# Performance work log

Measured on AMD Instinct MI355X. Metric: run time of the kernel, lower is better.

Reference implementation:

```python
import jax, jax.numpy as jnp
import numpy as np

N_NODES = 10000
N_EDGES = 640000
D_IN = 128
D_OUT = 128


def setup_inputs() -> dict:
    key = jax.random.key(0)
    ks = jax.random.split(key, 8)
    x = jax.random.normal(ks[0], (N_NODES, D_IN), dtype=jnp.float32)
    edge_index = jax.random.randint(ks[1], (2, N_EDGES), 0, N_NODES, dtype=jnp.int64)
    batch = jnp.zeros((N_NODES,), dtype=jnp.int64)
    s_in = 1.0 / np.sqrt(D_IN)
    s_out = 1.0 / np.sqrt(D_OUT)
    W_lin = jax.random.uniform(ks[2], (D_OUT, D_IN), jnp.float32, -s_in, s_in)
    b_lin = jax.random.uniform(ks[3], (D_OUT,), jnp.float32, -s_in, s_in)
    W_gate = jax.random.uniform(ks[4], (1, D_IN), jnp.float32, -s_in, s_in)
    b_gate = jax.random.uniform(ks[5], (1,), jnp.float32, -s_in, s_in)
    W_out = jax.random.uniform(ks[6], (D_OUT, D_OUT), jnp.float32, -s_out, s_out)
    b_out = jax.random.uniform(ks[7], (D_OUT,), jnp.float32, -s_out, s_out)
    return {"x": x, "edge_index": edge_index, "batch": batch,
            "W_lin": W_lin, "b_lin": b_lin, "W_gate": W_gate, "b_gate": b_gate,
            "W_out": W_out, "b_out": b_out}


def reference(x, edge_index, batch, W_lin, b_lin, W_gate, b_gate, W_out, b_out):
    row, col = edge_index[0], edge_index[1]
    n = x.shape[0]
    messages = x[col]                                      # [E, D_IN] gather
    gate = messages @ W_gate.T + b_gate                    # [E, 1]
    h = messages @ W_lin.T + b_lin                         # [E, D_OUT]
    # segment softmax over edges grouped by destination node (row)
    g = gate[:, 0]
    seg_max = jax.ops.segment_max(g, row, num_segments=n)  # -inf for empty segments (never gathered)
    e = jnp.exp(g - seg_max[row])
    denom = jax.ops.segment_sum(e, row, num_segments=n) + 1e-16
    attn = (e / denom[row])[:, None]                       # [E, 1]
    pooled = jax.ops.segment_sum(attn * h, row, num_segments=n)  # [N, D_OUT]
    return pooled @ W_out.T + b_out
```

## Files before the change

### kernel.cpp

```cpp
#include <hip/hip_runtime.h>
#include <math.h>

#define N_NODES_C 10000
#define N_EDGES_C 640000
#define DIM 128
#define NB 625
#define CAP 1344
#define CHUNK 4096
#define KPT 16
#define GATE_BLOCKS 2500
#define WC_BLOCKS 64
#define SCAT_BLOCKS ((N_EDGES_C + CHUNK - 1) / CHUNK)

__device__ __forceinline__ unsigned pack_bf16x2(float a, float b) {
    unsigned ua = __float_as_uint(a);
    unsigned ub = __float_as_uint(b);
    ua = (ua + 0x7FFFu + ((ua >> 16) & 1u)) >> 16;
    ub = (ub + 0x7FFFu + ((ub >> 16) & 1u)) >> 16;
    return ua | (ub << 16);
}
#define BF_LO(u) __uint_as_float((u) << 16)
#define BF_HI(u) __uint_as_float((u) & 0xFFFF0000u)

__global__ void prep_scatter_kernel(const float* __restrict__ x,
                                    const float* __restrict__ w_gate,
                                    const float* __restrict__ b_gate,
                                    const float* __restrict__ W_out,
                                    const float* __restrict__ W_lin,
                                    const float* __restrict__ b_lin,
                                    const int* __restrict__ row,
                                    const int* __restrict__ col,
                                    float* __restrict__ eg,
                                    unsigned* __restrict__ xh,
                                    int* __restrict__ bucket_fill,
                                    int* __restrict__ edata_b,
                                    float* __restrict__ WcT,
                                    float* __restrict__ bc,
                                    int n, int nE) {
    __shared__ int   histS[NB];
    __shared__ int   lbaseS[NB];
    __shared__ float wrow[2][DIM];
    __shared__ float red[2][DIM];
    int tid = threadIdx.x;
    int bx  = blockIdx.x;

    if (bx < GATE_BLOCKS) {
        int gid  = bx * 256 + tid;
        int wid  = gid >> 6;
        int lane = tid & 63;
        if (wid < n) {
            const float2* xr = (const float2*)(x + (size_t)wid * DIM);
            float2 a = xr[lane];
            float2 b = ((const float2*)w_gate)[lane];
            xh[(size_t)wid * 64 + lane] = pack_bf16x2(a.x, a.y);
            float v = a.x * b.x + a.y * b.y;
            #pragma unroll
            for (int off = 32; off; off >>= 1) v += __shfl_xor(v, off);
            if (lane == 0) eg[wid] = expf(v + b_gate[0]);
        }
    } else if (bx < GATE_BLOCKS + WC_BLOCKS) {
        int grp = tid >> 7;
        int i   = tid & 127;
        int o   = (bx - GATE_BLOCKS) * 2 + grp;
        wrow[grp][i] = W_out[o * DIM + i];
        __syncthreads();
        float acc = 0.f;
        #pragma unroll 8
        for (int k = 0; k < DIM; k++) acc += wrow[grp][k] * W_lin[k * DIM + i];
        WcT[i * DIM + o] = acc;
        red[grp][i] = wrow[grp][i] * b_lin[i];
        __syncthreads();
        for (int off = 64; off; off >>= 1) {
            if (i < off) red[grp][i] += red[grp][i + off];
            __syncthreads();
        }
        if (i == 0) bc[o] = red[grp][0];
    } else {
        int sb = bx - GATE_BLOCKS - WC_BLOCKS;
        for (int i = tid; i < NB; i += 256) histS[i] = 0;
        __syncthreads();

        int start = sb * CHUNK;
        int bkt[KPT], rnk[KPT], cl[KPT];
        #pragma unroll
        for (int k = 0; k < KPT; k++) {
            int e = start + k * 256 + tid;
            if (e < nE) {
                int r = row[e];
                int b = r >> 4;
                bkt[k] = b;
                cl[k]  = ((r & 15) << 16) | col[e];
                rnk[k] = atomicAdd(&histS[b], 1);
            } else { bkt[k] = -1; rnk[k] = 0; cl[k] = 0; }
        }
        __syncthreads();
        for (int i = tid; i < NB; i += 256)
            lbaseS[i] = histS[i] ? atomicAdd(&bucket_fill[i], histS[i]) : 0;
        __syncthreads();
        #pragma unroll
        for (int k = 0; k < KPT; k++) {
            if (bkt[k] >= 0) {
                int p = lbaseS[bkt[k]] + rnk[k];
                if (p < CAP)
                    edata_b[(size_t)bkt[k] * CAP + p] = cl[k];
            }
        }
    }
}

__global__ __launch_bounds__(512)
void bagg_kernel(const unsigned* __restrict__ xh,
                 const float* __restrict__ eg,
                 const int* __restrict__ edata_b,
                 const int* __restrict__ bucket_fill,
                 const float* __restrict__ WcT,
                 const float* __restrict__ bc,
                 const float* __restrict__ b_out,
                 float* __restrict__ out, int n) {
    __shared__ float aggT[16 * DIM];
    __shared__ float egS[N_NODES_C];
    __shared__ int  cntS[16], baseS[16], curS[16];
    __shared__ float sS[16];
    int* srt = (int*)aggT;

    int b   = blockIdx.x;
    int tid = threadIdx.x;
    int cnt = bucket_fill[b]; if (cnt > CAP) cnt = CAP;
    const int* eb = edata_b + (size_t)b * CAP;

    {
        const float4* eg4 = (const float4*)eg;
        float4* egS4 = (float4*)egS;
        #pragma unroll
        for (int k = 0; k < 5; k++) {
            int i = tid + k * 512;
            if (i < N_NODES_C / 4) egS4[i] = eg4[i];
        }
    }
    if (tid < 16) cntS[tid] = 0;
    __syncthreads();

    int rec[3];
    #pragma unroll
    for (int k = 0; k < 3; k++) {
        int j = tid + k * 512;
        rec[k] = (j < cnt) ? eb[j] : -1;
        if (rec[k] >= 0) atomicAdd(&cntS[rec[k] >> 16], 1);
    }
    __syncthreads();

    if (tid < 16) {
        int v = cntS[tid];
        int s = v;
        #pragma unroll
        for (int off = 1; off < 16; off <<= 1) {
            int t = __shfl_up(s, off);
            if (tid >= off) s += t;
        }
        baseS[tid] = s - v;
        curS[tid]  = s - v;
    }
    __syncthreads();

    #pragma unroll
    for (int k = 0; k < 3; k++) {
        if (rec[k] >= 0) {
            int p = atomicAdd(&curS[rec[k] >> 16], 1);
            srt[p] = rec[k] & 0xFFFF;
        }
    }
    __syncthreads();

    int l  = tid >> 5;
    int sl = tid & 31;
    int beg = baseS[l];
    int end = beg + cntS[l];

    float4 acc = make_float4(0.f, 0.f, 0.f, 0.f);
    float denom = 0.f;
    int j = beg;
    for (; j + 8 <= end; j += 8) {
        int c0 = srt[j];     int c1 = srt[j + 1];
        int c2 = srt[j + 2]; int c3 = srt[j + 3];
        int c4 = srt[j + 4]; int c5 = srt[j + 5];
        int c6 = srt[j + 6]; int c7 = srt[j + 7];
        float e0 = egS[c0], e1 = egS[c1], e2 = egS[c2], e3 = egS[c3];
        float e4 = egS[c4], e5 = egS[c5], e6 = egS[c6], e7 = egS[c7];
        uint2 u0 = ((const uint2*)(xh + (size_t)c0 * 64))[sl];
        uint2 u1 = ((const uint2*)(xh + (size_t)c1 * 64))[sl];
        uint2 u2 = ((const uint2*)(xh + (size_t)c2 * 64))[sl];
        uint2 u3 = ((const uint2*)(xh + (size_t)c3 * 64))[sl];
        uint2 u4 = ((const uint2*)(xh + (size_t)c4 * 64))[sl];
        uint2 u5 = ((const uint2*)(xh + (size_t)c5 * 64))[sl];
        uint2 u6 = ((const uint2*)(xh + (size_t)c6 * 64))[sl];
        uint2 u7 = ((const uint2*)(xh + (size_t)c7 * 64))[sl];
        denom += ((e0 + e1) + (e2 + e3)) + ((e4 + e5) + (e6 + e7));
        acc.x += e0 * BF_LO(u0.x) + e1 * BF_LO(u1.x) + e2 * BF_LO(u2.x) + e3 * BF_LO(u3.x)
               + e4 * BF_LO(u4.x) + e5 * BF_LO(u5.x) + e6 * BF_LO(u6.x) + e7 * BF_LO(u7.x);
        acc.y += e0 * BF_HI(u0.x) + e1 * BF_HI(u1.x) + e2 * BF_HI(u2.x) + e3 * BF_HI(u3.x)
               + e4 * BF_HI(u4.x) + e5 * BF_HI(u5.x) + e6 * BF_HI(u6.x) + e7 * BF_HI(u7.x);
        acc.z += e0 * BF_LO(u0.y) + e1 * BF_LO(u1.y) + e2 * BF_LO(u2.y) + e3 * BF_LO(u3.y)
               + e4 * BF_LO(u4.y) + e5 * BF_LO(u5.y) + e6 * BF_LO(u6.y) + e7 * BF_LO(u7.y);
        acc.w += e0 * BF_HI(u0.y) + e1 * BF_HI(u1.y) + e2 * BF_HI(u2.y) + e3 * BF_HI(u3.y)
               + e4 * BF_HI(u4.y) + e5 * BF_HI(u5.y) + e6 * BF_HI(u6.y) + e7 * BF_HI(u7.y);
    }
    for (; j < end; j++) {
        int c = srt[j];
        float ev = egS[c];
        uint2 u = ((const uint2*)(xh + (size_t)c * 64))[sl];
        denom += ev;
        acc.x += ev * BF_LO(u.x); acc.y += ev * BF_HI(u.x);
        acc.z += ev * BF_LO(u.y); acc.w += ev * BF_HI(u.y);
    }
    __syncthreads();

    float inv = 1.f / (denom + 1e-16f);
    {
        float4 r;
        r.x = acc.x * inv; r.y = acc.y * inv;
        r.z = acc.z * inv; r.w = acc.w * inv;
        ((float4*)(aggT + l * DIM))[sl] = r;
        if (sl == 0) sS[l] = denom * inv;
    }
    __syncthreads();

    int grp = tid >> 7;
    int o   = tid & 127;
    int l0  = grp * 4;
    float bcv = bc[o];
    float bov = b_out[o];
    float a0 = 0.f, a1 = 0.f, a2 = 0.f, a3 = 0.f;
    const float* t0 = aggT + (l0 + 0) * DIM;
    const float* t1 = aggT + (l0 + 1) * DIM;
    const float* t2 = aggT + (l0 + 2) * DIM;
    const float* t3 = aggT + (l0 + 3) * DIM;
    #pragma unroll 4
    for (int i = 0; i < DIM; i++) {
        float w = WcT[i * DIM + o];
        a0 += w * t0[i];
        a1 += w * t1[i];
        a2 += w * t2[i];
        a3 += w * t3[i];
    }
    int nodeBase = (b << 4) + l0;
    if (nodeBase + 0 < n) out[(size_t)(nodeBase + 0) * DIM + o] = a0 + sS[l0 + 0] * bcv + bov;
    if (nodeBase + 1 < n) out[(size_t)(nodeBase + 1) * DIM + o] = a1 + sS[l0 + 1] * bcv + bov;
    if (nodeBase + 2 < n) out[(size_t)(nodeBase + 2) * DIM + o] = a2 + sS[l0 + 2] * bcv + bov;
    if (nodeBase + 3 < n) out[(size_t)(nodeBase + 3) * DIM + o] = a3 + sS[l0 + 3] * bcv + bov;
}

extern "C" void kernel_launch(void* const* d_in, const int* in_sizes, int n_in,
                              void* d_out, int out_size, void* d_ws, size_t ws_size,
                              hipStream_t stream) {
    const float* x      = (const float*)d_in[0];
    const int*   eidx   = (const int*)d_in[1];
    const float* W_lin  = (const float*)d_in[3];
    const float* b_lin  = (const float*)d_in[4];
    const float* W_gate = (const float*)d_in[5];
    const float* b_gate = (const float*)d_in[6];
    const float* W_out  = (const float*)d_in[7];
    const float* b_out  = (const float*)d_in[8];
    float* out = (float*)d_out;

    const int n  = N_NODES_C;
    const int nE = N_EDGES_C;
    const int* row = eidx;
    const int* col = eidx + nE;

    char* ws = (char*)d_ws;
    size_t off = 0;
    auto carve = [&](size_t bytes) -> char* {
        char* p = ws + off;
        off += (bytes + 255) & ~(size_t)255;
        return p;
    };
    float*    eg          = (float*)   carve((size_t)n * 4);
    unsigned* xh          = (unsigned*)carve((size_t)n * 64 * 4);
    int*      bucket_fill = (int*)     carve((size_t)NB * 4);
    int*      edata_b     = (int*)     carve((size_t)NB * CAP * 4);
    float*    WcT         = (float*)   carve((size_t)DIM * DIM * 4);
    float*    bc          = (float*)   carve((size_t)DIM * 4);

    hipMemsetAsync(bucket_fill, 0, (size_t)NB * 4, stream);
    prep_scatter_kernel<<<GATE_BLOCKS + WC_BLOCKS + SCAT_BLOCKS, 256, 0, stream>>>(
        x, W_gate, b_gate, W_out, W_lin, b_lin, row, col,
        eg, xh, bucket_fill, edata_b, WcT, bc, n, nE);
    bagg_kernel<<<NB, 512, 0, stream>>>(
        xh, eg, edata_b, bucket_fill, WcT, bc, b_out, out, n);
}
```

Before: 53.49 us.

## Scatter edges into coarse 128-node buckets; filter per fine block in aggregation

The edge scatter now uses 79 coarse buckets of 128 destination nodes instead of 625 fine buckets, which cuts global atomics and improves write locality in the prep kernel. Each aggregation block now scans the whole coarse region, about 8x more records, and keeps only the edges for its 16-node sub-bucket. The gather loop is also reworked so two half-wavefronts each load uint4 (8 bf16 values) per neighbour and combine with shuffles. The final 128x128 projection now stages WcT through LDS in chunks that reuse the egS buffer. The trade-off is fewer scatter atomics and wider loads against extra redundant region reads in every aggregation block.

```diff
diff --git a/kernel.cpp b/kernel.cpp
--- a/kernel.cpp
+++ b/kernel.cpp
@@ -4,8 +4,9 @@
 #define N_NODES_C 10000
 #define N_EDGES_C 640000
 #define DIM 128
-#define NB 625
-#define CAP 1344
+#define NFINE 625
+#define NCOARSE 79
+#define CAPC 8704
 #define CHUNK 4096
 #define KPT 16
 #define GATE_BLOCKS 2500
@@ -32,13 +33,13 @@
                                     const int* __restrict__ col,
                                     float* __restrict__ eg,
                                     unsigned* __restrict__ xh,
-                                    int* __restrict__ bucket_fill,
-                                    int* __restrict__ edata_b,
+                                    int* __restrict__ cursor,
+                                    int* __restrict__ region,
                                     float* __restrict__ WcT,
                                     float* __restrict__ bc,
                                     int n, int nE) {
-    __shared__ int   histS[NB];
-    __shared__ int   lbaseS[NB];
+    __shared__ int   histS[NCOARSE];
+    __shared__ int   lbaseS[NCOARSE];
     __shared__ float wrow[2][DIM];
     __shared__ float red[2][DIM];
     int tid = threadIdx.x;
@@ -77,7 +78,7 @@
         if (i == 0) bc[o] = red[grp][0];
     } else {
         int sb = bx - GATE_BLOCKS - WC_BLOCKS;
-        for (int i = tid; i < NB; i += 256) histS[i] = 0;
+        if (tid < NCOARSE) histS[tid] = 0;
         __syncthreads();
 
         int start = sb * CHUNK;
@@ -87,22 +88,22 @@
             int e = start + k * 256 + tid;
             if (e < nE) {
                 int r = row[e];
-                int b = r >> 4;
+                int b = r >> 7;
                 bkt[k] = b;
-                cl[k]  = ((r & 15) << 16) | col[e];
+                cl[k]  = ((r & 127) << 16) | col[e];
                 rnk[k] = atomicAdd(&histS[b], 1);
             } else { bkt[k] = -1; rnk[k] = 0; cl[k] = 0; }
         }
         __syncthreads();
-        for (int i = tid; i < NB; i += 256)
-            lbaseS[i] = histS[i] ? atomicAdd(&bucket_fill[i], histS[i]) : 0;
+        if (tid < NCOARSE)
+            lbaseS[tid] = histS[tid] ? atomicAdd(&cursor[tid], histS[tid]) : 0;
         __syncthreads();
         #pragma unroll
         for (int k = 0; k < KPT; k++) {
             if (bkt[k] >= 0) {
                 int p = lbaseS[bkt[k]] + rnk[k];
-                if (p < CAP)
-                    edata_b[(size_t)bkt[k] * CAP + p] = cl[k];
+                if (p < CAPC)
+                    region[(size_t)bkt[k] * CAPC + p] = cl[k];
             }
         }
     }
@@ -111,22 +112,22 @@
 __global__ __launch_bounds__(512)
 void bagg_kernel(const unsigned* __restrict__ xh,
                  const float* __restrict__ eg,
-                 const int* __restrict__ edata_b,
-                 const int* __restrict__ bucket_fill,
+                 const int* __restrict__ region,
+                 const int* __restrict__ cursor,
                  const float* __restrict__ WcT,
                  const float* __restrict__ bc,
                  const float* __restrict__ b_out,
                  float* __restrict__ out, int n) {
+    __shared__ float egS[N_NODES_C];
     __shared__ float aggT[16 * DIM];
-    __shared__ float egS[N_NODES_C];
     __shared__ int  cntS[16], baseS[16], curS[16];
     __shared__ float sS[16];
     int* srt = (int*)aggT;
 
     int b   = blockIdx.x;
     int tid = threadIdx.x;
-    int cnt = bucket_fill[b]; if (cnt > CAP) cnt = CAP;
-    const int* eb = edata_b + (size_t)b * CAP;
+    int c   = b >> 3;
+    int sub = b & 7;
 
     {
         const float4* eg4 = (const float4*)eg;
@@ -140,12 +141,13 @@
     if (tid < 16) cntS[tid] = 0;
     __syncthreads();
 
-    int rec[3];
-    #pragma unroll
-    for (int k = 0; k < 3; k++) {
-        int j = tid + k * 512;
-        rec[k] = (j < cnt) ? eb[j] : -1;
-        if (rec[k] >= 0) atomicAdd(&cntS[rec[k] >> 16], 1);
+    int fill = cursor[c]; if (fill > CAPC) fill = CAPC;
+    const int* reg = region + (size_t)c * CAPC;
+
+    for (int j = tid; j < fill; j += 512) {
+        int rec = reg[j];
+        int l7  = rec >> 16;
+        if ((l7 >> 4) == sub) atomicAdd(&cntS[l7 & 15], 1);
     }
     __syncthreads();
 
@@ -162,91 +164,116 @@
     }
     __syncthreads();
 
-    #pragma unroll
-    for (int k = 0; k < 3; k++) {
-        if (rec[k] >= 0) {
-            int p = atomicAdd(&curS[rec[k] >> 16], 1);
-            srt[p] = rec[k] & 0xFFFF;
-        }
-    }
-    __syncthreads();
-
-    int l  = tid >> 5;
-    int sl = tid & 31;
+    for (int j = tid; j < fill; j += 512) {
+        int rec = reg[j];
+        int l7  = rec >> 16;
+        if ((l7 >> 4) == sub) {
+            int p = atomicAdd(&curS[l7 & 15], 1);
+            if (p < 2048) srt[p] = rec & 0xFFFF;
+        }
+    }
+    __syncthreads();
+
+    int l   = tid >> 5;
+    int q   = (tid >> 4) & 1;
+    int s16 = tid & 15;
     int beg = baseS[l];
     int end = beg + cntS[l];
 
-    float4 acc = make_float4(0.f, 0.f, 0.f, 0.f);
-    float denom = 0.f;
+    float a0=0.f,a1=0.f,a2=0.f,a3=0.f,a4=0.f,a5=0.f,a6=0.f,a7=0.f;
+    float dl = 0.f;
     int j = beg;
     for (; j + 8 <= end; j += 8) {
-        int c0 = srt[j];     int c1 = srt[j + 1];
-        int c2 = srt[j + 2]; int c3 = srt[j + 3];
-        int c4 = srt[j + 4]; int c5 = srt[j + 5];
-        int c6 = srt[j + 6]; int c7 = srt[j + 7];
-        float e0 = egS[c0], e1 = egS[c1], e2 = egS[c2], e3 = egS[c3];
-        float e4 = egS[c4], e5 = egS[c5], e6 = egS[c6], e7 = egS[c7];
-        uint2 u0 = ((const uint2*)(xh + (size_t)c0 * 64))[sl];
-        uint2 u1 = ((const uint2*)(xh + (size_t)c1 * 64))[sl];
-        uint2 u2 = ((const uint2*)(xh + (size_t)c2 * 64))[sl];
-        uint2 u3 = ((const uint2*)(xh + (size_t)c3 * 64))[sl];
-        uint2 u4 = ((const uint2*)(xh + (size_t)c4 * 64))[sl];
-        uint2 u5 = ((const uint2*)(xh + (size_t)c5 * 64))[sl];
-        uint2 u6 = ((const uint2*)(xh + (size_t)c6 * 64))[sl];
-        uint2 u7 = ((const uint2*)(xh + (size_t)c7 * 64))[sl];
-        denom += ((e0 + e1) + (e2 + e3)) + ((e4 + e5) + (e6 + e7));
-        acc.x += e0 * BF_LO(u0.x) + e1 * BF_LO(u1.x) + e2 * BF_LO(u2.x) + e3 * BF_LO(u3.x)
-               + e4 * BF_LO(u4.x) + e5 * BF_LO(u5.x) + e6 * BF_LO(u6.x) + e7 * BF_LO(u7.x);
-        acc.y += e0 * BF_HI(u0.x) + e1 * BF_HI(u1.x) + e2 * BF_HI(u2.x) + e3 * BF_HI(u3.x)
-               + e4 * BF_HI(u4.x) + e5 * BF_HI(u5.x) + e6 * BF_HI(u6.x) + e7 * BF_HI(u7.x);
-        acc.z += e0 * BF_LO(u0.y) + e1 * BF_LO(u1.y) + e2 * BF_LO(u2.y) + e3 * BF_LO(u3.y)
-               + e4 * BF_LO(u4.y) + e5 * BF_LO(u5.y) + e6 * BF_LO(u6.y) + e7 * BF_LO(u7.y);
-        acc.w += e0 * BF_HI(u0.y) + e1 * BF_HI(u1.y) + e2 * BF_HI(u2.y) + e3 * BF_HI(u3.y)
-               + e4 * BF_HI(u4.y) + e5 * BF_HI(u5.y) + e6 * BF_HI(u6.y) + e7 * BF_HI(u7.y);
-    }
-    for (; j < end; j++) {
-        int c = srt[j];
-        float ev = egS[c];
-        uint2 u = ((const uint2*)(xh + (size_t)c * 64))[sl];
-        denom += ev;
-        acc.x += ev * BF_LO(u.x); acc.y += ev * BF_HI(u.x);
-        acc.z += ev * BF_LO(u.y); acc.w += ev * BF_HI(u.y);
-    }
-    __syncthreads();
-
-    float inv = 1.f / (denom + 1e-16f);
-    {
-        float4 r;
-        r.x = acc.x * inv; r.y = acc.y * inv;
-        r.z = acc.z * inv; r.w = acc.w * inv;
-        ((float4*)(aggT + l * DIM))[sl] = r;
-        if (sl == 0) sS[l] = denom * inv;
-    }
-    __syncthreads();
-
+        #pragma unroll
+        for (int p = 0; p < 4; p++) {
+            int   cc = srt[j + 2 * p + q];
+            float e  = egS[cc];
+            uint4 u  = ((const uint4*)(xh + (size_t)cc * 64))[s16];
+            dl += e;
+            a0 += e * BF_LO(u.x); a1 += e * BF_HI(u.x);
+            a2 += e * BF_LO(u.y); a3 += e * BF_HI(u.y);
+            a4 += e * BF_LO(u.z); a5 += e * BF_HI(u.z);
+            a6 += e * BF_LO(u.w); a7 += e * BF_HI(u.w);
+        }
+    }
+    for (; j + 2 <= end; j += 2) {
+        int   cc = srt[j + q];
+        float e  = egS[cc];
+        uint4 u  = ((const uint4*)(xh + (size_t)cc * 64))[s16];
+        dl += e;
+        a0 += e * BF_LO(u.x); a1 += e * BF_HI(u.x);
+        a2 += e * BF_LO(u.y); a3 += e * BF_HI(u.y);
+        a4 += e * BF_LO(u.z); a5 += e * BF_HI(u.z);
+        a6 += e * BF_LO(u.w); a7 += e * BF_HI(u.w);
+    }
+    if (j < end) {
+        int   cc = srt[j];
+        float e  = q ? 0.f : egS[cc];
+        uint4 u  = ((const uint4*)(xh + (size_t)cc * 64))[s16];
+        dl += e;
+        a0 += e * BF_LO(u.x); a1 += e * BF_HI(u.x);
+        a2 += e * BF_LO(u.y); a3 += e * BF_HI(u.y);
+        a4 += e * BF_LO(u.z); a5 += e * BF_HI(u.z);
+        a6 += e * BF_LO(u.w); a7 += e * BF_HI(u.w);
+    }
+
+    a0 += __shfl_xor(a0, 16); a1 += __shfl_xor(a1, 16);
+    a2 += __shfl_xor(a2, 16); a3 += __shfl_xor(a3, 16);
+    a4 += __shfl_xor(a4, 16); a5 += __shfl_xor(a5, 16);
+    a6 += __shfl_xor(a6, 16); a7 += __shfl_xor(a7, 16);
+    #pragma unroll
+    for (int off = 16; off; off >>= 1) dl += __shfl_xor(dl, off);
+    float denom = dl * 0.0625f;
+    float inv   = 1.f / (denom + 1e-16f);
+
+    __syncthreads();
+    if (q == 0) {
+        float4 r0 = make_float4(a0 * inv, a1 * inv, a2 * inv, a3 * inv);
+        float4 r1 = make_float4(a4 * inv, a5 * inv, a6 * inv, a7 * inv);
+        float4* dst = (float4*)(aggT + l * DIM + 8 * s16);
+        dst[0] = r0;
+        dst[1] = r1;
+        if (s16 == 0) sS[l] = denom * inv;
+    }
+    __syncthreads();
+
+    float* lds_w = egS;
     int grp = tid >> 7;
     int o   = tid & 127;
     int l0  = grp * 4;
     float bcv = bc[o];
     float bov = b_out[o];
-    float a0 = 0.f, a1 = 0.f, a2 = 0.f, a3 = 0.f;
-    const float* t0 = aggT + (l0 + 0) * DIM;
-    const float* t1 = aggT + (l0 + 1) * DIM;
-    const float* t2 = aggT + (l0 + 2) * DIM;
-    const float* t3 = aggT + (l0 + 3) * DIM;
-    #pragma unroll 4
-    for (int i = 0; i < DIM; i++) {
-        float w = WcT[i * DIM + o];
-        a0 += w * t0[i];
-        a1 += w * t1[i];
-        a2 += w * t2[i];
-        a3 += w * t3[i];
-    }
+    float o0 = 0.f, o1 = 0.f, o2 = 0.f, o3 = 0.f;
+
+    for (int ch = 0; ch < 4; ch++) {
+        #pragma unroll
+        for (int k = 0; k < 8; k++)
+            lds_w[k * 512 + tid] = WcT[ch * 4096 + k * 512 + tid];
+        __syncthreads();
+        #pragma unroll 2
+        for (int i4 = 0; i4 < 8; i4++) {
+            int i = ch * 32 + i4 * 4;
+            float4 t0 = *(const float4*)(aggT + (l0 + 0) * DIM + i);
+            float4 t1 = *(const float4*)(aggT + (l0 + 1) * DIM + i);
+            float4 t2 = *(const float4*)(aggT + (l0 + 2) * DIM + i);
+            float4 t3 = *(const float4*)(aggT + (l0 + 3) * DIM + i);
+            float w0 = lds_w[(i4 * 4 + 0) * 128 + o];
+            float w1 = lds_w[(i4 * 4 + 1) * 128 + o];
+            float w2 = lds_w[(i4 * 4 + 2) * 128 + o];
+            float w3 = lds_w[(i4 * 4 + 3) * 128 + o];
+            o0 += w0 * t0.x + w1 * t0.y + w2 * t0.z + w3 * t0.w;
+            o1 += w0 * t1.x + w1 * t1.y + w2 * t1.z + w3 * t1.w;
+            o2 += w0 * t2.x + w1 * t2.y + w2 * t2.z + w3 * t2.w;
+            o3 += w0 * t3.x + w1 * t3.y + w2 * t3.z + w3 * t3.w;
+        }
+        __syncthreads();
+    }
+
     int nodeBase = (b << 4) + l0;
-    if (nodeBase + 0 < n) out[(size_t)(nodeBase + 0) * DIM + o] = a0 + sS[l0 + 0] * bcv + bov;
-    if (nodeBase + 1 < n) out[(size_t)(nodeBase + 1) * DIM + o] = a1 + sS[l0 + 1] * bcv + bov;
-    if (nodeBase + 2 < n) out[(size_t)(nodeBase + 2) * DIM + o] = a2 + sS[l0 + 2] * bcv + bov;
-    if (nodeBase + 3 < n) out[(size_t)(nodeBase + 3) * DIM + o] = a3 + sS[l0 + 3] * bcv + bov;
+    if (nodeBase + 0 < n) out[(size_t)(nodeBase + 0) * DIM + o] = o0 + sS[l0 + 0] * bcv + bov;
+    if (nodeBase + 1 < n) out[(size_t)(nodeBase + 1) * DIM + o] = o1 + sS[l0 + 1] * bcv + bov;
+    if (nodeBase + 2 < n) out[(size_t)(nodeBase + 2) * DIM + o] = o2 + sS[l0 + 2] * bcv + bov;
+    if (nodeBase + 3 < n) out[(size_t)(nodeBase + 3) * DIM + o] = o3 + sS[l0 + 3] * bcv + bov;
 }
 
 extern "C" void kernel_launch(void* const* d_in, const int* in_sizes, int n_in,
@@ -274,17 +301,17 @@
         off += (bytes + 255) & ~(size_t)255;
         return p;
     };
-    float*    eg          = (float*)   carve((size_t)n * 4);
-    unsigned* xh          = (unsigned*)carve((size_t)n * 64 * 4);
-    int*      bucket_fill = (int*)     carve((size_t)NB * 4);
-    int*      edata_b     = (int*)     carve((size_t)NB * CAP * 4);
-    float*    WcT         = (float*)   carve((size_t)DIM * DIM * 4);
-    float*    bc          = (float*)   carve((size_t)DIM * 4);
-
-    hipMemsetAsync(bucket_fill, 0, (size_t)NB * 4, stream);
+    float*    eg     = (float*)   carve((size_t)n * 4);
+    unsigned* xh     = (unsigned*)carve((size_t)n * 64 * 4);
+    int*      cursor = (int*)     carve((size_t)NCOARSE * 4);
+    int*      region = (int*)     carve((size_t)NCOARSE * CAPC * 4);
+    float*    WcT    = (float*)   carve((size_t)DIM * DIM * 4);
+    float*    bc     = (float*)   carve((size_t)DIM * 4);
+
+    hipMemsetAsync(cursor, 0, (size_t)NCOARSE * 4, stream);
     prep_scatter_kernel<<<GATE_BLOCKS + WC_BLOCKS + SCAT_BLOCKS, 256, 0, stream>>>(
         x, W_gate, b_gate, W_out, W_lin, b_lin, row, col,
-        eg, xh, bucket_fill, edata_b, WcT, bc, n, nE);
-    bagg_kernel<<<NB, 512, 0, stream>>>(
-        xh, eg, edata_b, bucket_fill, WcT, bc, b_out, out, n);
+        eg, xh, cursor, region, WcT, bc, n, nE);
+    bagg_kernel<<<NFINE, 512, 0, stream>>>(
+        xh, eg, region, cursor, WcT, bc, b_out, out, n);
 }
```

New measurement: 60.43 us. 13.0% more time.
